# Performance work log

Hardware: AMD Instinct MI355X
Metric: run time of the kernel (lower is better)

Reference implementation:

```python
import jax, jax.numpy as jnp
import numpy as np

B, K_LEN, Q_LEN, E, H = 16, 2048, 1024, 512, 8


def _layer_norm(x, g, b, eps=1e-5):
    mu = jnp.mean(x, axis=-1, keepdims=True)
    var = jnp.mean(jnp.square(x - mu), axis=-1, keepdims=True)
    return (x - mu) * jax.lax.rsqrt(var + eps) * g + b


def setup_inputs() -> dict:
    key = jax.random.key(0)
    ks = jax.random.split(key, 8)
    w = lambda k, sh: (jax.random.normal(k, sh, dtype=jnp.float32) * 0.02)
    return {
        "x_key": jax.random.normal(ks[0], (B, K_LEN, E), dtype=jnp.float32),
        "in_proj_w": w(ks[1], (3 * E, E)),
        "in_proj_b": jnp.zeros((3 * E,), jnp.float32),
        "out_w": w(ks[2], (E, E)),
        "out_b": jnp.zeros((E,), jnp.float32),
        "ln1_g": jnp.ones((E,), jnp.float32),
        "ln1_b": jnp.zeros((E,), jnp.float32),
        "w1": w(ks[3], (E, E)),
        "b1": jnp.zeros((E,), jnp.float32),
        "w2": w(ks[4], (E, E)),
        "b2": jnp.zeros((E,), jnp.float32),
        "ln2_g": jnp.ones((E,), jnp.float32),
        "ln2_b": jnp.zeros((E,), jnp.float32),
        "query_length": Q_LEN,
        "key_padding_mask": jax.random.bernoulli(ks[5], 0.2, (B, K_LEN)),
    }


def _attn_mask(key_length, query_length, key_padding_mask):
    # True = masked.  triu causal part, shared across batch/heads.
    triu = jnp.triu(jnp.ones((key_length, key_length), dtype=bool), k=1)
    m = triu[-query_length:]  # [Q, K]
    m = m[None] | key_padding_mask[:, None, :]  # [B, Q, K]
    not_eye = ~jnp.eye(key_length, dtype=bool)[-query_length:]  # [Q, K]
    m = m & not_eye[None]  # diagonal (self) always attendable
    return m  # [B, Q, K]; identical across heads


def reference(x_key, in_proj_w, in_proj_b, out_w, out_b,
              ln1_g, ln1_b, w1, b1, w2, b2, ln2_g, ln2_b,
              query_length, key_padding_mask):
    b, k_len, e = x_key.shape
    dh = e // H
    q_len = query_length

    # pad key_padding_mask on the left with its first column (static shapes)
    L = key_padding_mask.shape[1]
    if L < k_len:
        pad = jnp.repeat(key_padding_mask[:, :1], k_len - L, axis=1)
        key_padding_mask = jnp.concatenate([pad, key_padding_mask], axis=1)

    query = x_key[:, -q_len:]  # [B, Q, E]

    wq, wk, wv = jnp.split(in_proj_w, 3, axis=0)
    bq, bk, bv = jnp.split(in_proj_b, 3, axis=0)
    q = (query @ wq.T + bq).reshape(b, q_len, H, dh).transpose(0, 2, 1, 3)
    k = (x_key @ wk.T + bk).reshape(b, k_len, H, dh).transpose(0, 2, 1, 3)
    v = (x_key @ wv.T + bv).reshape(b, k_len, H, dh).transpose(0, 2, 1, 3)

    scores = jnp.einsum('bhqd,bhkd->bhqk', q, k) * (dh ** -0.5)
    mask = _attn_mask(k_len, q_len, key_padding_mask)  # [B, Q, K]
    scores = jnp.where(mask[:, None], -jnp.inf, scores)
    attn = jax.nn.softmax(scores, axis=-1)  # [B, H, Q, K]

    ctx = jnp.einsum('bhqk,bhkd->bhqd', attn, v)
    ctx = ctx.transpose(0, 2, 1, 3).reshape(b, q_len, e)
    attn_out = ctx @ out_w.T + out_b

    t = _layer_norm(attn_out + query, ln1_g, ln1_b)
    ff = jax.nn.relu(t @ w1.T + b1) @ w2.T + b2
    output = _layer_norm(ff + t, ln2_g, ln2_b)
    attn_weights = attn.mean(axis=1)  # head-averaged, torch default
    return output, attn_weights
```

## Files before the change

### kernel.cpp

```cpp
#include <hip/hip_runtime.h>

typedef unsigned short u16t;
typedef __attribute__((ext_vector_type(4))) unsigned short us4;
typedef __attribute__((ext_vector_type(8))) unsigned short us8;
typedef __attribute__((ext_vector_type(8))) short s8v;
typedef __attribute__((ext_vector_type(4))) float f4v;

#define NB 16
#define KL 2048
#define QL 1024
#define EE 512
#define NH 8
#define DH 64

#define QSCALE 0.18033688011112042f

__device__ __forceinline__ float b2f(u16t u) {
  return __uint_as_float(((unsigned)u) << 16);
}
__device__ __forceinline__ u16t f2b(float f) {
  unsigned u = __float_as_uint(f);
  u += 0x7fffu + ((u >> 16) & 1u);
  return (u16t)(u >> 16);
}
__device__ __forceinline__ u16t f2b_fast(float f) {
  return (u16t)((__float_as_uint(f) + 0x8000u) >> 16);
}
__device__ __forceinline__ float fexp2(float x) {
  return __builtin_amdgcn_exp2f(x);
}

__device__ __forceinline__ int detect_mode(const int* kpm_i) {
  bool small = true, oddzero = true, evenone = false;
  for (int i = 0; i < 64; ++i) {
    unsigned v = (unsigned)kpm_i[i];
    if (v > 1u) small = false;
    if ((i & 1) && v != 0u) oddzero = false;
    if (!(i & 1) && v == 1u) evenone = true;
  }
  return !small ? 0 : ((oddzero && evenone) ? 2 : 1);
}

__global__ __launch_bounds__(256) void cvt_weights(
    const float* __restrict__ wi, const float* __restrict__ wo,
    const float* __restrict__ wf1, const float* __restrict__ wf2,
    u16t* __restrict__ dst) {
  int i = blockIdx.x * 256 + threadIdx.x;
  const float* src;
  int j;
  if (i < 196608) { src = wi; j = i; }
  else if (i < 262144) { src = wo; j = i - 196608; }
  else if (i < 327680) { src = wf1; j = i - 262144; }
  else { src = wf2; j = i - 327680; }
  float4 v = ((const float4*)src)[j];
  us4 o = {f2b(v.x), f2b(v.y), f2b(v.z), f2b(v.w)};
  *(us4*)&dst[i * 4] = o;
}

__global__ __launch_bounds__(256) void mfma_gemm_qkv(
    const float* __restrict__ A, const u16t* __restrict__ Wb,
    const float* __restrict__ bias, u16t* __restrict__ q_ws,
    u16t* __restrict__ k_ws, u16t* __restrict__ v_ws) {
  const int Kd = EE;
  __shared__ u16t Alds[128 * 40];
  __shared__ u16t Blds[128 * 40];
  const int t = threadIdx.x;
  const int n0 = blockIdx.x * 128, m0 = blockIdx.y * 128;
  const int lane = t & 63, w = t >> 6;
  const int col = lane & 15, quad = lane >> 4;
  const int wm = w & 1, wn = w >> 1;

  const int arow = t >> 1, ahalf = t & 1;
  const int wrow = t >> 1, wseg = t & 1;

  f4v acc[4][4] = {};

  for (int kc = 0; kc < Kd; kc += 32) {
    const float* ap = &A[(size_t)(m0 + arow) * Kd + kc + ahalf * 16];
    float4 f0 = ((const float4*)ap)[0];
    float4 f1 = ((const float4*)ap)[1];
    float4 f2_ = ((const float4*)ap)[2];
    float4 f3 = ((const float4*)ap)[3];
    const u16t* wp = &Wb[(size_t)(n0 + wrow) * Kd + kc + wseg * 16];
    us8 w0 = *(const us8*)wp;
    us8 w1 = *(const us8*)(wp + 8);
    __syncthreads();
    us8 o0 = {f2b(f0.x), f2b(f0.y), f2b(f0.z), f2b(f0.w),
              f2b(f1.x), f2b(f1.y), f2b(f1.z), f2b(f1.w)};
    us8 o1 = {f2b(f2_.x), f2b(f2_.y), f2b(f2_.z), f2b(f2_.w),
              f2b(f3.x), f2b(f3.y), f2b(f3.z), f2b(f3.w)};
    *(us8*)&Alds[arow * 40 + ahalf * 16] = o0;
    *(us8*)&Alds[arow * 40 + ahalf * 16 + 8] = o1;
    *(us8*)&Blds[wrow * 40 + wseg * 16] = w0;
    *(us8*)&Blds[wrow * 40 + wseg * 16 + 8] = w1;
    __syncthreads();
    s8v af[4], bf[4];
#pragma unroll
    for (int mt = 0; mt < 4; ++mt)
      af[mt] = *(s8v*)&Alds[(wm * 64 + mt * 16 + col) * 40 + quad * 8];
#pragma unroll
    for (int nt = 0; nt < 4; ++nt)
      bf[nt] = *(s8v*)&Blds[(wn * 64 + nt * 16 + col) * 40 + quad * 8];
#pragma unroll
    for (int mt = 0; mt < 4; ++mt)
#pragma unroll
      for (int nt = 0; nt < 4; ++nt)
        acc[mt][nt] = __builtin_amdgcn_mfma_f32_16x16x32_bf16(
            af[mt], bf[nt], acc[mt][nt], 0, 0, 0);
  }

  float bv[4];
#pragma unroll
  for (int nt = 0; nt < 4; ++nt) bv[nt] = bias[n0 + wn * 64 + nt * 16 + col];

#pragma unroll
  for (int nt = 0; nt < 4; ++nt) {
    int n = n0 + wn * 64 + nt * 16 + col;
    int sec = n >> 9, hh = (n >> 6) & 7, dd = n & 63;
#pragma unroll
    for (int mt = 0; mt < 4; ++mt)
#pragma unroll
      for (int r = 0; r < 4; ++r) {
        int m = m0 + wm * 64 + mt * 16 + quad * 4 + r;
        int bb_ = m >> 11, pos = m & 2047;
        float val = acc[mt][nt][r] + bv[nt];
        if (sec == 0) {
          if (pos >= QL)
            q_ws[((bb_ * NH + hh) * QL + pos - QL) * DH + dd] =
                f2b(val * QSCALE);
        } else if (sec == 1) {
          k_ws[((bb_ * NH + hh) * KL + pos) * DH + dd] = f2b(val);
        } else {
          v_ws[((bb_ * NH + hh) * DH + dd) * KL + pos] = f2b(val);
        }
      }
  }
}

__global__ __launch_bounds__(256) void mfma_gemm_bias(
    const u16t* __restrict__ A, const u16t* __restrict__ Wb,
    const float* __restrict__ bias, u16t* __restrict__ C, int M, int N,
    int Kd, int relu) {
  __shared__ u16t Alds[128 * 40];
  __shared__ u16t Blds[128 * 40];
  const int t = threadIdx.x;
  const int n0 = blockIdx.x * 128, m0 = blockIdx.y * 128;
  const int lane = t & 63, w = t >> 6;
  const int col = lane & 15, quad = lane >> 4;
  const int wm = w & 1, wn = w >> 1;
  const int row = t >> 1, seg = t & 1;

  f4v acc[4][4] = {};

  for (int kc = 0; kc < Kd; kc += 32) {
    const u16t* ap = &A[(size_t)(m0 + row) * Kd + kc + seg * 16];
    us8 a0 = *(const us8*)ap;
    us8 a1 = *(const us8*)(ap + 8);
    const u16t* wp = &Wb[(size_t)(n0 + row) * Kd + kc + seg * 16];
    us8 w0 = *(const us8*)wp;
    us8 w1 = *(const us8*)(wp + 8);
    __syncthreads();
    *(us8*)&Alds[row * 40 + seg * 16] = a0;
    *(us8*)&Alds[row * 40 + seg * 16 + 8] = a1;
    *(us8*)&Blds[row * 40 + seg * 16] = w0;
    *(us8*)&Blds[row * 40 + seg * 16 + 8] = w1;
    __syncthreads();
    s8v af[4], bf[4];
#pragma unroll
    for (int mt = 0; mt < 4; ++mt)
      af[mt] = *(s8v*)&Alds[(wm * 64 + mt * 16 + col) * 40 + quad * 8];
#pragma unroll
    for (int nt = 0; nt < 4; ++nt)
      bf[nt] = *(s8v*)&Blds[(wn * 64 + nt * 16 + col) * 40 + quad * 8];
#pragma unroll
    for (int mt = 0; mt < 4; ++mt)
#pragma unroll
      for (int nt = 0; nt < 4; ++nt)
        acc[mt][nt] = __builtin_amdgcn_mfma_f32_16x16x32_bf16(
            af[mt], bf[nt], acc[mt][nt], 0, 0, 0);
  }

  float bv[4];
#pragma unroll
  for (int nt = 0; nt < 4; ++nt) bv[nt] = bias[n0 + wn * 64 + nt * 16 + col];

#pragma unroll
  for (int mt = 0; mt < 4; ++mt)
#pragma unroll
    for (int nt = 0; nt < 4; ++nt) {
      int n = n0 + wn * 64 + nt * 16 + col;
#pragma unroll
      for (int r = 0; r < 4; ++r) {
        int m = m0 + wm * 64 + mt * 16 + quad * 4 + r;
        float v = acc[mt][nt][r] + bv[nt];
        if (relu) v = fmaxf(v, 0.f);
        C[(size_t)m * N + n] = f2b(v);
      }
    }
}

__global__ __launch_bounds__(256, 2) void attn_fwd(
    const u16t* __restrict__ qw, const u16t* __restrict__ kw,
    const u16t* __restrict__ vw, const int* kpm_i, const unsigned char* kpm_b,
    u16t* __restrict__ ctx_out, float* __restrict__ l_ws) {
  const int q0 = blockIdx.x * 32;
  const int bh = blockIdx.y;
  const int b = bh >> 3, h = bh & 7;
  const int t = threadIdx.x;
  const int lane = t & 63, w = t >> 6;
  const int col = lane & 15, quad = lane >> 4;

  __shared__ unsigned char padb[KL];
  __shared__ __align__(16) char ubuf[32768];
  u16t (*plds)[2][16][72] = (u16t (*)[2][16][72])ubuf;
  float (*ctxm)[32][64] = (float (*)[32][64])ubuf;
  __shared__ float lsum[4][32];
  __shared__ float Lrow[32];
  __shared__ int mode_s;

  if (t == 0) mode_s = detect_mode(kpm_i);
  __syncthreads();
  const int mode = mode_s;
  for (int i = t; i < KL; i += 256) {
    int idx = b * KL + i;
    padb[i] = (mode == 0)
                  ? (kpm_b[idx] != 0)
                  : (mode == 1 ? (kpm_i[idx] != 0) : (kpm_i[2 * idx] != 0));
  }
  __syncthreads();

  s8v qa[2][2];
#pragma unroll
  for (int st = 0; st < 2; ++st)
#pragma unroll
    for (int hf = 0; hf < 2; ++hf)
      qa[st][hf] = *(const s8v*)&qw[(bh * QL + q0 + st * 16 + col) * DH +
                                    quad * 8 + 32 * hf];

  const f4v zf = {0.f, 0.f, 0.f, 0.f};
  const s8v ones = {16256, 16256, 16256, 16256,
                    16256, 16256, 16256, 16256};

  f4v cacc[2][4];
  f4v lacc[2];
#pragma unroll
  for (int st = 0; st < 2; ++st) {
    lacc[st] = zf;
#pragma unroll
    for (int dt = 0; dt < 4; ++dt) cacc[st][dt] = zf;
  }

  const int qmaxk = q0 + 31 + QL;
  const size_t kbase = (size_t)bh * KL * DH;
  const size_t vbase = (size_t)bh * DH * KL;

  int kc = w * 64;
  s8v kcur[4][2];
#pragma unroll
  for (int tt = 0; tt < 4; ++tt) {
    const u16t* kp = &kw[kbase + (size_t)(kc + tt * 16 + col) * DH + quad * 8];
    kcur[tt][0] = *(const s8v*)kp;
    kcur[tt][1] = *(const s8v*)(kp + 32);
  }

  while (true) {
    s8v vcur[4][2];
#pragma unroll
    for (int dt = 0; dt < 4; ++dt) {
      const u16t* vp = &vw[vbase + (size_t)(dt * 16 + col) * KL + kc + quad * 8];
      vcur[dt][0] = *(const s8v*)vp;
      vcur[dt][1] = *(const s8v*)(vp + 32);
    }
    const int kcn = kc + 256;
    const bool more = (kcn <= qmaxk);
    s8v knxt[4][2];
    if (more) {
#pragma unroll
      for (int tt = 0; tt < 4; ++tt) {
        const u16t* kp =
            &kw[kbase + (size_t)(kcn + tt * 16 + col) * DH + quad * 8];
        knxt[tt][0] = *(const s8v*)kp;
        knxt[tt][1] = *(const s8v*)(kp + 32);
      }
    }

    f4v sts[2][4];
#pragma unroll
    for (int tt = 0; tt < 4; ++tt)
#pragma unroll
      for (int st = 0; st < 2; ++st) {
        f4v c = __builtin_amdgcn_mfma_f32_16x16x32_bf16(qa[st][0],
                                                        kcur[tt][0], zf, 0, 0, 0);
        sts[st][tt] = __builtin_amdgcn_mfma_f32_16x16x32_bf16(
            qa[st][1], kcur[tt][1], c, 0, 0, 0);
      }

    const bool interior = (kc + 63 < q0 + QL);

#pragma unroll
    for (int st = 0; st < 2; ++st) {
      if (interior) {
#pragma unroll
        for (int tt = 0; tt < 4; ++tt) {
          bool pad = padb[kc + tt * 16 + col] != 0;
#pragma unroll
          for (int r = 0; r < 4; ++r) {
            float v = pad ? -1.0e30f : sts[st][tt][r];
            float p = fexp2(v);
            plds[w][st][quad * 4 + r][tt * 16 + col] = f2b_fast(p);
          }
        }
      } else {
#pragma unroll
        for (int tt = 0; tt < 4; ++tt) {
          int key = kc + tt * 16 + col;
          bool pad = padb[key] != 0;
#pragma unroll
          for (int r = 0; r < 4; ++r) {
            int qrow = q0 + st * 16 + quad * 4 + r;
            bool al = (key <= qrow + QL) && (!pad || key == qrow + QL);
            float v = al ? sts[st][tt][r] : -1.0e30f;
            float p = fexp2(v);
            plds[w][st][quad * 4 + r][tt * 16 + col] = f2b_fast(p);
          }
        }
      }
    }

    s8v pa[2][2];
#pragma unroll
    for (int st = 0; st < 2; ++st)
#pragma unroll
      for (int hf = 0; hf < 2; ++hf)
        pa[st][hf] = *(const s8v*)&plds[w][st][col][hf * 32 + quad * 8];
#pragma unroll
    for (int st = 0; st < 2; ++st) {
      lacc[st] = __builtin_amdgcn_mfma_f32_16x16x32_bf16(pa[st][0], ones,
                                                         lacc[st], 0, 0, 0);
      lacc[st] = __builtin_amdgcn_mfma_f32_16x16x32_bf16(pa[st][1], ones,
                                                         lacc[st], 0, 0, 0);
    }
#pragma unroll
    for (int dt = 0; dt < 4; ++dt)
#pragma unroll
      for (int st = 0; st < 2; ++st) {
        cacc[st][dt] = __builtin_amdgcn_mfma_f32_16x16x32_bf16(
            pa[st][0], vcur[dt][0], cacc[st][dt], 0, 0, 0);
        cacc[st][dt] = __builtin_amdgcn_mfma_f32_16x16x32_bf16(
            pa[st][1], vcur[dt][1], cacc[st][dt], 0, 0, 0);
      }

    if (!more) break;
    kc = kcn;
#pragma unroll
    for (int tt = 0; tt < 4; ++tt) {
      kcur[tt][0] = knxt[tt][0];
      kcur[tt][1] = knxt[tt][1];
    }
  }

  __syncthreads();
#pragma unroll
  for (int st = 0; st < 2; ++st)
#pragma unroll
    for (int dt = 0; dt < 4; ++dt)
#pragma unroll
      for (int r = 0; r < 4; ++r)
        ctxm[w][st * 16 + quad * 4 + r][dt * 16 + col] = cacc[st][dt][r];
  if (col == 0) {
#pragma unroll
    for (int st = 0; st < 2; ++st)
#pragma unroll
      for (int r = 0; r < 4; ++r)
        lsum[w][st * 16 + quad * 4 + r] = lacc[st][r];
  }
  __syncthreads();
  if (t < 32) {
    int q = t;
    float L = lsum[0][q] + lsum[1][q] + lsum[2][q] + lsum[3][q];
    float inv = 1.0f / L;
    Lrow[q] = inv;
    l_ws[bh * QL + q0 + q] = 0.125f * inv;
  }
  __syncthreads();
  for (int i = t; i < 2048; i += 256) {
    int q = i >> 6, d = i & 63;
    float v = ctxm[0][q][d] + ctxm[1][q][d] + ctxm[2][q][d] + ctxm[3][q][d];
    v *= Lrow[q];
    ctx_out[(b * QL + q0 + q) * EE + h * DH + d] = f2b(v);
  }
}

__global__ __launch_bounds__(256, 2) void attn_aw(
    const u16t* __restrict__ qw, const u16t* __restrict__ kw,
    const int* kpm_i, const unsigned char* kpm_b,
    const float* __restrict__ l_ws, float* __restrict__ aw_out) {
  const int q0 = blockIdx.x * 32;
  const int k0 = blockIdx.y * 128;
  const int b = blockIdx.z;
  const int t = threadIdx.x;
  const int lane = t & 63, w = t >> 6;
  const int col = lane & 15, quad = lane >> 4;
  const int qmaxk = q0 + 31 + QL;

  if (k0 > qmaxk) {
    for (int i = t; i < 32 * 128; i += 256) {
      int q = i >> 7, c = i & 127;
      aw_out[(b * QL + q0 + q) * KL + k0 + c] = 0.f;
    }
    return;
  }

  __shared__ unsigned char padb[128];
  __shared__ int mode_s;
  if (t == 0) mode_s = detect_mode(kpm_i);
  __syncthreads();
  const int mode = mode_s;
  if (t < 128) {
    int idx = b * KL + k0 + t;
    padb[t] = (mode == 0)
                  ? (kpm_b[idx] != 0)
                  : (mode == 1 ? (kpm_i[idx] != 0) : (kpm_i[2 * idx] != 0));
  }
  __syncthreads();

  const bool interior = (k0 + 127 < q0 + QL);

  const int kt = k0 + w * 32;
  const f4v zf = {0.f, 0.f, 0.f, 0.f};
  f4v acc[2][2];
#pragma unroll
  for (int st = 0; st < 2; ++st)
#pragma unroll
    for (int tt = 0; tt < 2; ++tt) acc[st][tt] = zf;

  bool padl[2];
  padl[0] = padb[kt + col - k0] != 0;
  padl[1] = padb[kt + 16 + col - k0] != 0;

  auto load_frags = [&](int hh, s8v qa[2][2], s8v kb[2][2]) {
    const int bh = b * NH + hh;
#pragma unroll
    for (int st = 0; st < 2; ++st)
#pragma unroll
      for (int hf = 0; hf < 2; ++hf)
        qa[st][hf] = *(const s8v*)&qw[(bh * QL + q0 + st * 16 + col) * DH +
                                      quad * 8 + 32 * hf];
#pragma unroll
    for (int tt = 0; tt < 2; ++tt) {
      const u16t* kp = &kw[((size_t)bh * KL + kt + tt * 16 + col) * DH +
                           quad * 8];
      kb[tt][0] = *(const s8v*)kp;
      kb[tt][1] = *(const s8v*)(kp + 32);
    }
  };
  auto load_ml = [&](int hh, float Li[2][4]) {
    const int bh = b * NH + hh;
#pragma unroll
    for (int st = 0; st < 2; ++st) {
      float4 l4 = *(const float4*)&l_ws[bh * QL + q0 + st * 16 + quad * 4];
      Li[st][0] = l4.x; Li[st][1] = l4.y; Li[st][2] = l4.z; Li[st][3] = l4.w;
    }
  };
  auto compute = [&](const s8v qa[2][2], const s8v kb[2][2],
                     const float Li[2][4]) {
#pragma unroll
    for (int tt = 0; tt < 2; ++tt) {
      const int ktt = kt + tt * 16;
      if (ktt > qmaxk) continue;
      const bool pad = padl[tt];
      const int key = ktt + col;
#pragma unroll
      for (int st = 0; st < 2; ++st) {
        f4v c = __builtin_amdgcn_mfma_f32_16x16x32_bf16(qa[st][0], kb[tt][0],
                                                        zf, 0, 0, 0);
        c = __builtin_amdgcn_mfma_f32_16x16x32_bf16(qa[st][1], kb[tt][1], c,
                                                    0, 0, 0);
        if (interior) {
#pragma unroll
          for (int r = 0; r < 4; ++r) {
            float e = fexp2(c[r]);
            float li = pad ? 0.f : Li[st][r];
            acc[st][tt][r] = fmaf(e, li, acc[st][tt][r]);
          }
        } else {
#pragma unroll
          for (int r = 0; r < 4; ++r) {
            int qrow = q0 + st * 16 + quad * 4 + r;
            bool al = (key <= qrow + QL) && (!pad || key == qrow + QL);
            float e = fexp2(c[r]);
            float li = al ? Li[st][r] : 0.f;
            acc[st][tt][r] = fmaf(e, li, acc[st][tt][r]);
          }
        }
      }
    }
  };

  s8v qaA[2][2], kbA[2][2], qaB[2][2], kbB[2][2];
  float LiA[2][4], LiB[2][4];

  load_frags(0, qaA, kbA);
  load_ml(0, LiA);
#pragma unroll
  for (int hp = 0; hp < NH; hp += 2) {
    load_frags(hp + 1, qaB, kbB);
    load_ml(hp + 1, LiB);
    compute(qaA, kbA, LiA);
    if (hp + 2 < NH) {
      load_frags(hp + 2, qaA, kbA);
      load_ml(hp + 2, LiA);
    }
    compute(qaB, kbB, LiB);
  }

#pragma unroll
  for (int st = 0; st < 2; ++st)
#pragma unroll
    for (int tt = 0; tt < 2; ++tt)
#pragma unroll
      for (int r = 0; r < 4; ++r)
        aw_out[(b * QL + q0 + st * 16 + quad * 4 + r) * KL + kt + tt * 16 +
               col] = acc[st][tt][r];
}

__global__ __launch_bounds__(256) void ln_res(
    const u16t* __restrict__ x, const u16t* __restrict__ res_b,
    const float* __restrict__ res_f, int res_is_xkey,
    const float* __restrict__ g, const float* __restrict__ bb,
    u16t* __restrict__ out_b, float* __restrict__ out_f, int out_f32) {
  __shared__ float red[4];
  int row = blockIdx.x;
  int t = threadIdx.x;
  int base = row * EE;
  float r0, r1;
  if (res_is_xkey) {
    int b = row >> 10, qq = row & 1023;
    int rbase = (b * KL + QL + qq) * EE;
    r0 = res_f[rbase + t];
    r1 = res_f[rbase + t + 256];
  } else {
    r0 = b2f(res_b[base + t]);
    r1 = b2f(res_b[base + t + 256]);
  }
  float a0 = b2f(x[base + t]) + r0;
  float a1 = b2f(x[base + t + 256]) + r1;
  float sv = a0 + a1;
#pragma unroll
  for (int off = 32; off > 0; off >>= 1) sv += __shfl_down(sv, off);
  if ((t & 63) == 0) red[t >> 6] = sv;
  __syncthreads();
  float mu = (red[0] + red[1] + red[2] + red[3]) * (1.0f / 512.0f);
  __syncthreads();
  float d0 = a0 - mu, d1 = a1 - mu;
  float vv = d0 * d0 + d1 * d1;
#pragma unroll
  for (int off = 32; off > 0; off >>= 1) vv += __shfl_down(vv, off);
  if ((t & 63) == 0) red[t >> 6] = vv;
  __syncthreads();
  float var = (red[0] + red[1] + red[2] + red[3]) * (1.0f / 512.0f);
  float rs = rsqrtf(fmaxf(var, 0.f) + 1e-5f);
  float o0 = d0 * rs * g[t] + bb[t];
  float o1 = d1 * rs * g[t + 256] + bb[t + 256];
  if (out_f32) {
    out_f[base + t] = o0;
    out_f[base + t + 256] = o1;
  } else {
    out_b[base + t] = f2b(o0);
    out_b[base + t + 256] = f2b(o1);
  }
}

extern "C" void kernel_launch(void* const* d_in, const int* in_sizes, int n_in,
                              void* d_out, int out_size, void* d_ws,
                              size_t ws_size, hipStream_t stream) {
  const float* x_key = (const float*)d_in[0];
  const float* in_proj_w = (const float*)d_in[1];
  const float* in_proj_b = (const float*)d_in[2];
  const float* out_w = (const float*)d_in[3];
  const float* out_b = (const float*)d_in[4];
  const float* ln1_g = (const float*)d_in[5];
  const float* ln1_b = (const float*)d_in[6];
  const float* w1 = (const float*)d_in[7];
  const float* b1 = (const float*)d_in[8];
  const float* w2 = (const float*)d_in[9];
  const float* b2 = (const float*)d_in[10];
  const float* ln2_g = (const float*)d_in[11];
  const float* ln2_b = (const float*)d_in[12];
  const void* kpm = d_in[14];

  float* out = (float*)d_out;
  u16t* ws = (u16t*)d_ws;

  u16t* wb_inproj = ws;
  u16t* wb_out = ws + 786432;
  u16t* wb_w1 = ws + 1048576;
  u16t* wb_w2 = ws + 1310720;
  u16t* q_ws = ws + 1572864;
  u16t* k_ws = ws + 9961472;
  u16t* v_ws = ws + 26738688;
  u16t* ctx_ws = ws + 43515904;
  float* l_ws = (float*)(ws + 51904512);
  u16t* ao_ws = q_ws;
  u16t* t_ws = ctx_ws;
  u16t* h1_ws = k_ws;
  u16t* ff_ws = v_ws;
  float* aw_out = out + (NB * QL * EE);

  cvt_weights<<<1536, 256, 0, stream>>>(in_proj_w, out_w, w1, w2, wb_inproj);
  mfma_gemm_qkv<<<dim3(12, 256), 256, 0, stream>>>(x_key, wb_inproj,
                                                   in_proj_b, q_ws, k_ws,
                                                   v_ws);
  attn_fwd<<<dim3(QL / 32, NB * NH), 256, 0, stream>>>(
      q_ws, k_ws, v_ws, (const int*)kpm, (const unsigned char*)kpm, ctx_ws,
      l_ws);
  attn_aw<<<dim3(QL / 32, KL / 128, NB), 256, 0, stream>>>(
      q_ws, k_ws, (const int*)kpm, (const unsigned char*)kpm, l_ws, aw_out);
  mfma_gemm_bias<<<dim3(4, 128), 256, 0, stream>>>(ctx_ws, wb_out, out_b,
                                                   ao_ws, NB * QL, EE, EE, 0);
  ln_res<<<NB * QL, 256, 0, stream>>>(ao_ws, nullptr, x_key, 1, ln1_g, ln1_b,
                                      t_ws, nullptr, 0);
  mfma_gemm_bias<<<dim3(4, 128), 256, 0, stream>>>(t_ws, wb_w1, b1, h1_ws,
                                                   NB * QL, EE, EE, 1);
  mfma_gemm_bias<<<dim3(4, 128), 256, 0, stream>>>(h1_ws, wb_w2, b2, ff_ws,
                                                   NB * QL, EE, EE, 0);
  ln_res<<<NB * QL, 256, 0, stream>>>(ff_ws, t_ws, nullptr, 0, ln2_g, ln2_b,
                                      nullptr, out, 1);
}
```

Before: 945.1 us.

## Raise attention occupancy, drop K prefetch, and remap blocks across heads

```diff
diff --git a/kernel.cpp b/kernel.cpp
--- a/kernel.cpp
+++ b/kernel.cpp
@@ -199,12 +199,14 @@
     }
 }
 
-__global__ __launch_bounds__(256, 2) void attn_fwd(
+__global__ __launch_bounds__(256, 4) void attn_fwd(
     const u16t* __restrict__ qw, const u16t* __restrict__ kw,
     const u16t* __restrict__ vw, const int* kpm_i, const unsigned char* kpm_b,
     u16t* __restrict__ ctx_out, float* __restrict__ l_ws) {
-  const int q0 = blockIdx.x * 32;
-  const int bh = blockIdx.y;
+  const int id = blockIdx.y * (int)gridDim.x + blockIdx.x;
+  const int j = id >> 3;
+  const int bh = (id & 7) * 16 + (j >> 5);
+  const int q0 = (j & 31) * 32;
   const int b = bh >> 3, h = bh & 7;
   const int t = threadIdx.x;
   const int lane = t & 63, w = t >> 6;
@@ -254,34 +256,24 @@
   const size_t kbase = (size_t)bh * KL * DH;
   const size_t vbase = (size_t)bh * DH * KL;
 
-  int kc = w * 64;
-  s8v kcur[4][2];
-#pragma unroll
-  for (int tt = 0; tt < 4; ++tt) {
-    const u16t* kp = &kw[kbase + (size_t)(kc + tt * 16 + col) * DH + quad * 8];
-    kcur[tt][0] = *(const s8v*)kp;
-    kcur[tt][1] = *(const s8v*)(kp + 32);
-  }
-
-  while (true) {
+  for (int i = 0; i < 8; ++i) {
+    const int kc = (i * 4 + w) * 64;
+    if (kc > qmaxk) break;
+
+    s8v kcur[4][2];
+#pragma unroll
+    for (int tt = 0; tt < 4; ++tt) {
+      const u16t* kp =
+          &kw[kbase + (size_t)(kc + tt * 16 + col) * DH + quad * 8];
+      kcur[tt][0] = *(const s8v*)kp;
+      kcur[tt][1] = *(const s8v*)(kp + 32);
+    }
     s8v vcur[4][2];
 #pragma unroll
     for (int dt = 0; dt < 4; ++dt) {
       const u16t* vp = &vw[vbase + (size_t)(dt * 16 + col) * KL + kc + quad * 8];
       vcur[dt][0] = *(const s8v*)vp;
       vcur[dt][1] = *(const s8v*)(vp + 32);
-    }
-    const int kcn = kc + 256;
-    const bool more = (kcn <= qmaxk);
-    s8v knxt[4][2];
-    if (more) {
-#pragma unroll
-      for (int tt = 0; tt < 4; ++tt) {
-        const u16t* kp =
-            &kw[kbase + (size_t)(kcn + tt * 16 + col) * DH + quad * 8];
-        knxt[tt][0] = *(const s8v*)kp;
-        knxt[tt][1] = *(const s8v*)(kp + 32);
-      }
     }
 
     f4v sts[2][4];
@@ -349,14 +341,6 @@
         cacc[st][dt] = __builtin_amdgcn_mfma_f32_16x16x32_bf16(
             pa[st][1], vcur[dt][1], cacc[st][dt], 0, 0, 0);
       }
-
-    if (!more) break;
-    kc = kcn;
-#pragma unroll
-    for (int tt = 0; tt < 4; ++tt) {
-      kcur[tt][0] = knxt[tt][0];
-      kcur[tt][1] = knxt[tt][1];
-    }
   }
 
   __syncthreads();
```

Result: slower. 1.017 ms (+7.6%).
